# Kernel optimization log

Measured on AMD Instinct MI355X. Metric: run time of the kernel, lower is better.

Reference implementation:

```python
import jax, jax.numpy as jnp
import numpy as np

TOP_K = 2
EPS = 1e-10


def setup_inputs() -> dict:
    key = jax.random.key(0)
    k1, k2, k3, k4 = jax.random.split(key, 4)
    B, S, H, E = 4, 2048, 1024, 8
    tokens = jax.random.normal(k1, (B, S, H), dtype=jnp.float32)
    router_w = jax.random.normal(k2, (E, H), dtype=jnp.float32) * (1.0 / np.sqrt(H))
    router_b = jax.random.normal(k3, (E,), dtype=jnp.float32) * 0.01
    expert_weights = jax.random.normal(k4, (E, H, H), dtype=jnp.float32) * (1.0 / np.sqrt(H))
    return {"tokens": tokens, "router_w": router_w, "router_b": router_b,
            "expert_weights": expert_weights}


def reference(tokens, router_w, router_b, expert_weights):
    B, S, H = tokens.shape
    E = expert_weights.shape[0]
    # Router (torch Linear: x @ W^T + b)
    logits = jnp.einsum('bsh,eh->bse', tokens, router_w) + router_b  # [B,S,E]
    probs = jax.nn.softmax(logits, axis=-1)
    top_p, top_i = jax.lax.top_k(probs, TOP_K)            # [B,S,K]
    w = top_p / (jnp.sum(top_p, axis=-1, keepdims=True) + EPS)  # normalized weights

    x = tokens.reshape(-1, H)                              # [N,H]
    idx = top_i.reshape(-1, TOP_K)                         # [N,K]
    wf = w.reshape(-1, TOP_K)                              # [N,K]

    # Expert GEMM: compute all experts then gather selected (dense, vectorized
    # equivalent of the sort/pad/grouped-GEMM dispatch; padded rows with
    # original_indices==-1 never contribute to the output).
    y_all = jnp.einsum('nh,ehd->ned', x, expert_weights)   # [N,E,H]
    y_k = jnp.take_along_axis(y_all, idx[:, :, None], axis=1)  # [N,K,H]

    out = jnp.einsum('nk,nkh->nh', wf, y_k)                # weighted combine
    acc = jnp.clip(jnp.sum(wf, axis=-1), EPS, None)        # weight accumulator
    out = (out / acc[:, None]).reshape(B, S, H)

    # epsilon scale tying output to normalized router probs (gradient path)
    scale = 1.0 + jnp.sum(w, axis=-1, keepdims=True) * EPS  # [B,S,1]
    return out * scale
```

## Files before the change

### kernel.cpp

```cpp
#include <hip/hip_runtime.h>
#include <stdint.h>

#define N_TOK 8192
#define H_DIM 1024
#define N_EXP 8
#define GEMM_GRID 1024

typedef __bf16 bf16x8 __attribute__((ext_vector_type(8)));
typedef float floatx4 __attribute__((ext_vector_type(4)));

typedef __attribute__((address_space(1))) void GV;
typedef __attribute__((address_space(3))) void LV;

static __device__ __forceinline__ unsigned short f2b(float f) {
    union { float f; unsigned int i; } v; v.f = f;
    unsigned int u = v.i;
    return (unsigned short)((u + 0x7FFFu + ((u >> 16) & 1u)) >> 16);
}
static __device__ __forceinline__ float b2f(unsigned short u) {
    union { unsigned int i; float f; } v; v.i = ((unsigned int)u) << 16; return v.f;
}

__global__ __launch_bounds__(256) void k_front(
    const float* __restrict__ tokens,
    const float* __restrict__ router_w,
    const float* __restrict__ router_b,
    const float* __restrict__ W,
    float* __restrict__ w_arr,
    unsigned short* __restrict__ tokb,
    unsigned short* __restrict__ Bp,
    int* __restrict__ cnt, int* __restrict__ bucket)
{
    const int t = threadIdx.x;

    if (blockIdx.x >= 1024) {
        const int idx = blockIdx.x - 1024;
        const int kg = idx & 127;
        const int e  = idx >> 7;
        const int d  = t * 4;
        const float* src = W + ((size_t)e * H_DIM + kg * 8) * H_DIM + d;
        float col[8][4];
#pragma unroll
        for (int j = 0; j < 8; ++j) {
            float4 v = *(const float4*)(src + (size_t)j * H_DIM);
            col[j][0] = v.x; col[j][1] = v.y; col[j][2] = v.z; col[j][3] = v.w;
        }
        unsigned short* dst = Bp + ((size_t)(e * 128 + kg) * H_DIM + d) * 8;
#pragma unroll
        for (int k = 0; k < 4; ++k) {
            unsigned short v[8];
#pragma unroll
            for (int j = 0; j < 8; ++j) v[j] = f2b(col[j][k]);
            *(uint4*)(dst + (size_t)k * 8) = *(uint4*)v;
        }
        return;
    }

    __shared__ int bcnt[N_EXP];
    __shared__ int blist[N_EXP][16];
    if (t < N_EXP) bcnt[t] = 0;
    __syncthreads();

    const int wv = t >> 6, lane = t & 63;
    const int n0 = blockIdx.x * 8 + wv * 2;

    float x0[16], x1[16];
    const float* xp0 = tokens + (size_t)n0 * H_DIM + lane * 16;
    const float* xp1 = xp0 + H_DIM;
#pragma unroll
    for (int i = 0; i < 4; ++i) {
        float4 v = *(const float4*)(xp0 + i * 4);
        x0[i * 4 + 0] = v.x; x0[i * 4 + 1] = v.y; x0[i * 4 + 2] = v.z; x0[i * 4 + 3] = v.w;
        float4 u = *(const float4*)(xp1 + i * 4);
        x1[i * 4 + 0] = u.x; x1[i * 4 + 1] = u.y; x1[i * 4 + 2] = u.z; x1[i * 4 + 3] = u.w;
    }
    {
        unsigned short xb[16];
#pragma unroll
        for (int j = 0; j < 16; ++j) xb[j] = f2b(x0[j]);
        unsigned short* dp = tokb + (size_t)n0 * H_DIM + lane * 16;
        *(uint4*)(dp) = *(uint4*)(xb); *(uint4*)(dp + 8) = *(uint4*)(xb + 8);
#pragma unroll
        for (int j = 0; j < 16; ++j) xb[j] = f2b(x1[j]);
        dp += H_DIM;
        *(uint4*)(dp) = *(uint4*)(xb); *(uint4*)(dp + 8) = *(uint4*)(xb + 8);
    }

    float a0[N_EXP], a1[N_EXP];
#pragma unroll
    for (int e = 0; e < N_EXP; ++e) {
        const float* wp = router_w + e * H_DIM + lane * 16;
        float s0 = 0.f, s1 = 0.f;
#pragma unroll
        for (int i = 0; i < 4; ++i) {
            float4 v = *(const float4*)(wp + i * 4);
            s0 += x0[i * 4 + 0] * v.x + x0[i * 4 + 1] * v.y + x0[i * 4 + 2] * v.z + x0[i * 4 + 3] * v.w;
            s1 += x1[i * 4 + 0] * v.x + x1[i * 4 + 1] * v.y + x1[i * 4 + 2] * v.z + x1[i * 4 + 3] * v.w;
        }
        a0[e] = s0; a1[e] = s1;
    }
#pragma unroll
    for (int e = 0; e < N_EXP; ++e) {
        float p = a0[e], q = a1[e];
#pragma unroll
        for (int off = 32; off > 0; off >>= 1) { p += __shfl_xor(p, off); q += __shfl_xor(q, off); }
        a0[e] = p; a1[e] = q;
    }

    if (lane == 0) {
#pragma unroll
        for (int k = 0; k < 2; ++k) {
            const int n = n0 + k;
            float lg[N_EXP];
#pragma unroll
            for (int e = 0; e < N_EXP; ++e) lg[e] = (k ? a1[e] : a0[e]) + router_b[e];
            int e0 = 0;
#pragma unroll
            for (int e = 1; e < N_EXP; ++e) if (lg[e] > lg[e0]) e0 = e;
            int e1 = -1;
#pragma unroll
            for (int e = 0; e < N_EXP; ++e) {
                if (e == e0) continue;
                if (e1 < 0 || lg[e] > lg[e1]) e1 = e;
            }
            float w0 = 1.f / (1.f + __expf(lg[e1] - lg[e0]));
            w_arr[n * 2] = w0;
            w_arr[n * 2 + 1] = 1.f - w0;
            int s0 = atomicAdd(&bcnt[e0], 1); blist[e0][s0] = 2 * n;
            int s1 = atomicAdd(&bcnt[e1], 1); blist[e1][s1] = 2 * n + 1;
        }
    }
    __syncthreads();

    if (t < N_EXP) {
        int c = bcnt[t];
        if (c > 0) {
            int base = atomicAdd(&cnt[t], c);
            int* dst = bucket + t * N_TOK + base;
            for (int i = 0; i < c; ++i) dst[i] = blist[t][i];
        }
    }
}

__global__ __launch_bounds__(256, 4) void k_gemm(
    const unsigned short* __restrict__ tokb,
    const unsigned short* __restrict__ Bp,
    const int* __restrict__ cnt, const int* __restrict__ bucket,
    unsigned short* __restrict__ Y, float* __restrict__ Yp, int split_ok)
{
    __shared__ __align__(16) unsigned short Asm[128 * 64];
    __shared__ __align__(16) unsigned short Bsm[8 * 128 * 8];
    __shared__ int rows[128];

    const int t = threadIdx.x;
    const int wv = t >> 6, lane = t & 63;
    const int w_row = wv >> 1, w_col = wv & 1;
    const int m_lane = lane & 15, quad = lane >> 4;
    const int r7 = m_lane & 7;
    const int p_sw = (lane & 7) ^ ((lane >> 3) & 7);

    int cs[N_EXP];
#pragma unroll
    for (int ee = 0; ee < N_EXP; ++ee) cs[ee] = cnt[ee];
    int T = 0;
#pragma unroll
    for (int ee = 0; ee < N_EXP; ++ee) T += (cs[ee] + 127) >> 7;

    const int x = blockIdx.x & 7;
    const int sblk = blockIdx.x >> 3;
    const int q = T >> 3, r = T & 7;
    const int tstart = (x < r) ? x * (q + 1) : r * (q + 1) + (x - r) * q;
    const int tcnt   = (x < r) ? (q + 1) : q;
    const int nloc   = tcnt * 8;

    int t0_tile, t0_nt, t0_k0, t0_k1, t0_os;
    int t1_tile = -1, t1_nt = 0, t1_k0 = 0, t1_k1 = 0, t1_os = -1;
    if (split_ok) {
        if (x < r && sblk < 32) {
            const int oi = sblk >> 2, qk = sblk & 3;
            t0_tile = tstart + 16; t0_nt = oi;
            t0_k0 = qk * 4; t0_k1 = qk * 4 + 4;
            t0_os = (x * 8 + oi) * 4 + qk;
            t1_tile = tstart + (sblk >> 3); t1_nt = sblk & 7;
            t1_k0 = 0; t1_k1 = 16; t1_os = -1;
        } else {
            t0_tile = tstart + (sblk >> 3); t0_nt = sblk & 7;
            t0_k0 = 0; t0_k1 = 16; t0_os = -1;
        }
    } else {
        t0_tile = tstart + (sblk >> 3); t0_nt = sblk & 7;
        t0_k0 = 0; t0_k1 = 16; t0_os = -1;
        if (sblk + 128 < nloc) {
            const int l2 = sblk + 128;
            t1_tile = tstart + (l2 >> 3); t1_nt = l2 & 7;
            t1_k0 = 0; t1_k1 = 16; t1_os = -1;
        }
    }

#pragma unroll 2
    for (int tk = 0; tk < 2; ++tk) {
        const int tile = tk ? t1_tile : t0_tile;
        if (tile < 0) continue;
        const int nt = tk ? t1_nt : t0_nt;
        const int k0 = tk ? t1_k0 : t0_k0;
        const int k1 = tk ? t1_k1 : t0_k1;
        const int os = tk ? t1_os : t0_os;

        int base = 0, e = 0, mt = 0;
#pragma unroll
        for (int ee = 0; ee < N_EXP; ++ee) {
            int te = (cs[ee] + 127) >> 7;
            if (tile >= base && tile < base + te) { e = ee; mt = tile - base; }
            base += te;
        }
        const int cnt_local = cs[e] - mt * 128;
        const int d0 = nt * 128;

        __syncthreads();
        if (t < 128)
            rows[t] = (t < cnt_local) ? bucket[e * N_TOK + mt * 128 + t] : -1;
        __syncthreads();

        const unsigned short* aptr[4];
#pragma unroll
        for (int i = 0; i < 4; ++i) {
            int rr = i * 32 + wv * 8 + (lane >> 3);
            int rid = rows[rr];
            int tok = (rid >= 0) ? (rid >> 1) : 0;
            aptr[i] = tokb + (size_t)tok * H_DIM + p_sw * 8;
        }
        const unsigned short* bbase = Bp
            + ((size_t)(e * 128 + (t >> 7)) * H_DIM + d0 + (t & 127)) * 8;

        floatx4 acc[4][4];
#pragma unroll
        for (int i = 0; i < 4; ++i)
#pragma unroll
            for (int j = 0; j < 4; ++j) acc[i][j] = (floatx4){0.f, 0.f, 0.f, 0.f};

        for (int kt = k0; kt < k1; ++kt) {
#pragma unroll
            for (int i = 0; i < 4; ++i) {
                __builtin_amdgcn_global_load_lds(
                    (GV*)(aptr[i] + kt * 64),
                    (LV*)(&Asm[i * 2048 + wv * 512]), 16, 0, 0);
                __builtin_amdgcn_global_load_lds(
                    (GV*)(bbase + (size_t)i * 16384 + (size_t)kt * 65536),
                    (LV*)(&Bsm[i * 2048 + wv * 512]), 16, 0, 0);
            }
            __syncthreads();

#pragma unroll
            for (int s = 0; s < 2; ++s) {
                bf16x8 a[4], b[4];
#pragma unroll
                for (int i = 0; i < 4; ++i) {
                    int row = w_row * 64 + i * 16 + m_lane;
                    a[i] = *(const bf16x8*)&Asm[row * 64 + ((s * 4 + quad) ^ r7) * 8];
                }
#pragma unroll
                for (int j = 0; j < 4; ++j)
                    b[j] = *(const bf16x8*)&Bsm[((s * 4 + quad) * 128 + w_col * 64 + j * 16 + m_lane) * 8];
#pragma unroll
                for (int i = 0; i < 4; ++i)
#pragma unroll
                    for (int j = 0; j < 4; ++j)
                        acc[i][j] = __builtin_amdgcn_mfma_f32_16x16x32_bf16(a[i], b[j], acc[i][j], 0, 0, 0);
            }
            __syncthreads();
        }

        if (os < 0) {
#pragma unroll
            for (int i = 0; i < 4; ++i) {
                const int lr_base = w_row * 64 + i * 16 + quad * 4;
#pragma unroll
                for (int reg = 0; reg < 4; ++reg) {
                    const int lr = lr_base + reg;
                    const int rid = rows[lr];
                    if (rid >= 0) {
                        unsigned short v[4];
#pragma unroll
                        for (int j = 0; j < 4; ++j) v[j] = f2b(acc[i][j][reg]);
                        *(uint2*)(Y + (size_t)rid * H_DIM + d0 + w_col * 64 + m_lane * 4) = *(uint2*)v;
                    }
                }
            }
        } else {
            float* dst = Yp + (size_t)os * 16384;
#pragma unroll
            for (int i = 0; i < 4; ++i) {
#pragma unroll
                for (int reg = 0; reg < 4; ++reg) {
                    const int lr = w_row * 64 + i * 16 + quad * 4 + reg;
                    float4 v = make_float4(acc[i][0][reg], acc[i][1][reg],
                                           acc[i][2][reg], acc[i][3][reg]);
                    *(float4*)(dst + lr * 128 + w_col * 64 + m_lane * 4) = v;
                }
            }
        }
    }
}

__global__ __launch_bounds__(256) void k_fix(
    const int* __restrict__ cnt, const int* __restrict__ bucket,
    const float* __restrict__ Yp, unsigned short* __restrict__ Y)
{
    int cs[N_EXP];
#pragma unroll
    for (int ee = 0; ee < N_EXP; ++ee) cs[ee] = cnt[ee];
    int T = 0;
#pragma unroll
    for (int ee = 0; ee < N_EXP; ++ee) T += (cs[ee] + 127) >> 7;
    const int q = T >> 3, r = T & 7;
    const int o = blockIdx.x;
    if (o >= 8 * r) return;
    const int x = o >> 3, oi = o & 7;
    const int tile = x * (q + 1) + q;
    const int nt = oi;

    int base = 0, e = 0, mt = 0;
#pragma unroll
    for (int ee = 0; ee < N_EXP; ++ee) {
        int te = (cs[ee] + 127) >> 7;
        if (tile >= base && tile < base + te) { e = ee; mt = tile - base; }
        base += te;
    }
    const int cnt_local = cs[e] - mt * 128;
    const int d0 = nt * 128;

    const int t = threadIdx.x;
    const int lr = t >> 1, half = t & 1;
    const int rid = (lr < cnt_local) ? bucket[e * N_TOK + mt * 128 + lr] : -1;
    if (rid < 0) return;

    const float* s = Yp + (size_t)o * 4 * 16384 + lr * 128 + half * 64;
    unsigned short* dst = Y + (size_t)rid * H_DIM + d0 + half * 64;
#pragma unroll
    for (int c = 0; c < 64; c += 8) {
        float sum[8];
#pragma unroll
        for (int k = 0; k < 8; ++k) sum[k] = s[c + k];
#pragma unroll
        for (int qk = 1; qk < 4; ++qk) {
            const float* sq = s + qk * 16384;
#pragma unroll
            for (int k = 0; k < 8; ++k) sum[k] += sq[c + k];
        }
        unsigned short v[8];
#pragma unroll
        for (int k = 0; k < 8; ++k) v[k] = f2b(sum[k]);
        *(uint4*)(dst + c) = *(uint4*)v;
    }
}

__global__ __launch_bounds__(256) void k_combine(
    const unsigned short* __restrict__ Y, const float* __restrict__ w_arr,
    float* __restrict__ out)
{
    __shared__ __align__(16) unsigned short Ys[4 * H_DIM];
    const int t = threadIdx.x;
    const int b = blockIdx.x;
    const int wv = t >> 6, lane = t & 63;
    const unsigned short* src = Y + (size_t)b * 4 * H_DIM;
#pragma unroll
    for (int r = 0; r < 2; ++r) {
        __builtin_amdgcn_global_load_lds(
            (GV*)(src + (size_t)r * 2048 + wv * 512 + lane * 8),
            (LV*)(&Ys[r * 2048 + wv * 512]), 16, 0, 0);
    }
    __syncthreads();

    const int tok = t >> 7;
    const int n = 2 * b + tok;
    const int d0 = (t & 127) * 8;
    const int seg = d0 >> 7;
    const int dseg = d0 & 127;
    const int wc = dseg >> 6;
    const int j  = (dseg >> 4) & 3;
    const int m0 = dseg & 15;
    const int sbase = tok * 2 * H_DIM + seg * 128 + wc * 64 + j;
    const float w0 = w_arr[2 * n], w1 = w_arr[2 * n + 1];

    float o[8];
#pragma unroll
    for (int k = 0; k < 8; ++k) {
        int s = sbase + (m0 + k) * 4;
        o[k] = w0 * b2f(Ys[s]) + w1 * b2f(Ys[s + H_DIM]);
    }
    float4* op = (float4*)(out + (size_t)n * H_DIM + d0);
    op[0] = make_float4(o[0], o[1], o[2], o[3]);
    op[1] = make_float4(o[4], o[5], o[6], o[7]);
}

extern "C" void kernel_launch(void* const* d_in, const int* in_sizes, int n_in,
                              void* d_out, int out_size, void* d_ws, size_t ws_size,
                              hipStream_t stream)
{
    const float* tokens   = (const float*)d_in[0];
    const float* router_w = (const float*)d_in[1];
    const float* router_b = (const float*)d_in[2];
    const float* W        = (const float*)d_in[3];
    float* out = (float*)d_out;

    char* ws = (char*)d_ws;
    int*   cnt    = (int*)(ws);
    float* w_arr  = (float*)(ws + 34816);
    int*   bucket = (int*)(ws + 100352);
    unsigned short* tokb = (unsigned short*)(ws + 362496);
    unsigned short* Bp   = (unsigned short*)(ws + 17139712);
    unsigned short* Y    = (unsigned short*)(ws + 33916928);
    float* Yp = (float*)(ws + 67471360);

    const int split_ok = (ws_size >= 82151424ull) ? 1 : 0;

    hipMemsetAsync(cnt, 0, N_EXP * sizeof(int), stream);
    k_front  <<<2048, 256, 0, stream>>>(tokens, router_w, router_b, W,
                                        w_arr, tokb, Bp, cnt, bucket);
    k_gemm   <<<GEMM_GRID, 256, 0, stream>>>(tokb, Bp, cnt, bucket, Y, Yp, split_ok);
    if (split_ok)
        k_fix<<<56, 256, 0, stream>>>(cnt, bucket, Yp, Y);
    k_combine<<<N_TOK * (H_DIM / 8) / 256, 256, 0, stream>>>(Y, w_arr, out);
}
```

Baseline: 190.0 us.

## Fold split-K partial reduction into combine kernel via per-row fix map

Removes the separate k_fix kernel that summed the four split-K fp32 partials and wrote them back to the bf16 Y buffer. The GEMM now records, for each row handled by a split tile, which partial buffer holds it. The combine kernel consults this map and reads and sums the fp32 partials directly instead of the bf16 Y values. This saves one kernel launch and a round-trip through Y, at the cost of an extra map read per token and a divergent branch in the combine kernel. As a side effect, split rows now skip bf16 rounding.

```diff
diff --git a/kernel.cpp b/kernel.cpp
--- a/kernel.cpp
+++ b/kernel.cpp
@@ -29,7 +29,8 @@
     float* __restrict__ w_arr,
     unsigned short* __restrict__ tokb,
     unsigned short* __restrict__ Bp,
-    int* __restrict__ cnt, int* __restrict__ bucket)
+    int* __restrict__ cnt, int* __restrict__ bucket,
+    int* __restrict__ fix_map)
 {
     const int t = threadIdx.x;
 
@@ -55,6 +56,8 @@
         }
         return;
     }
+
+    if (fix_map && t < 16) fix_map[blockIdx.x * 16 + t] = -1;
 
     __shared__ int bcnt[N_EXP];
     __shared__ int blist[N_EXP][16];
@@ -146,7 +149,8 @@
     const unsigned short* __restrict__ tokb,
     const unsigned short* __restrict__ Bp,
     const int* __restrict__ cnt, const int* __restrict__ bucket,
-    unsigned short* __restrict__ Y, float* __restrict__ Yp, int split_ok)
+    unsigned short* __restrict__ Y, float* __restrict__ Yp,
+    int* __restrict__ fix_map, int split_ok)
 {
     __shared__ __align__(16) unsigned short Asm[128 * 64];
     __shared__ __align__(16) unsigned short Bsm[8 * 128 * 8];
@@ -221,6 +225,9 @@
             rows[t] = (t < cnt_local) ? bucket[e * N_TOK + mt * 128 + t] : -1;
         __syncthreads();
 
+        if (os >= 0 && (os & 3) == 0 && t < 128 && rows[t] >= 0)
+            fix_map[rows[t]] = (x << 16) | t;
+
         const unsigned short* aptr[4];
 #pragma unroll
         for (int i = 0; i < 4; ++i) {
@@ -302,60 +309,9 @@
     }
 }
 
-__global__ __launch_bounds__(256) void k_fix(
-    const int* __restrict__ cnt, const int* __restrict__ bucket,
-    const float* __restrict__ Yp, unsigned short* __restrict__ Y)
-{
-    int cs[N_EXP];
-#pragma unroll
-    for (int ee = 0; ee < N_EXP; ++ee) cs[ee] = cnt[ee];
-    int T = 0;
-#pragma unroll
-    for (int ee = 0; ee < N_EXP; ++ee) T += (cs[ee] + 127) >> 7;
-    const int q = T >> 3, r = T & 7;
-    const int o = blockIdx.x;
-    if (o >= 8 * r) return;
-    const int x = o >> 3, oi = o & 7;
-    const int tile = x * (q + 1) + q;
-    const int nt = oi;
-
-    int base = 0, e = 0, mt = 0;
-#pragma unroll
-    for (int ee = 0; ee < N_EXP; ++ee) {
-        int te = (cs[ee] + 127) >> 7;
-        if (tile >= base && tile < base + te) { e = ee; mt = tile - base; }
-        base += te;
-    }
-    const int cnt_local = cs[e] - mt * 128;
-    const int d0 = nt * 128;
-
-    const int t = threadIdx.x;
-    const int lr = t >> 1, half = t & 1;
-    const int rid = (lr < cnt_local) ? bucket[e * N_TOK + mt * 128 + lr] : -1;
-    if (rid < 0) return;
-
-    const float* s = Yp + (size_t)o * 4 * 16384 + lr * 128 + half * 64;
-    unsigned short* dst = Y + (size_t)rid * H_DIM + d0 + half * 64;
-#pragma unroll
-    for (int c = 0; c < 64; c += 8) {
-        float sum[8];
-#pragma unroll
-        for (int k = 0; k < 8; ++k) sum[k] = s[c + k];
-#pragma unroll
-        for (int qk = 1; qk < 4; ++qk) {
-            const float* sq = s + qk * 16384;
-#pragma unroll
-            for (int k = 0; k < 8; ++k) sum[k] += sq[c + k];
-        }
-        unsigned short v[8];
-#pragma unroll
-        for (int k = 0; k < 8; ++k) v[k] = f2b(sum[k]);
-        *(uint4*)(dst + c) = *(uint4*)v;
-    }
-}
-
 __global__ __launch_bounds__(256) void k_combine(
     const unsigned short* __restrict__ Y, const float* __restrict__ w_arr,
+    const float* __restrict__ Yp, const int* __restrict__ fix_map,
     float* __restrict__ out)
 {
     __shared__ __align__(16) unsigned short Ys[4 * H_DIM];
@@ -379,15 +335,44 @@
     const int wc = dseg >> 6;
     const int j  = (dseg >> 4) & 3;
     const int m0 = dseg & 15;
-    const int sbase = tok * 2 * H_DIM + seg * 128 + wc * 64 + j;
+    const int tok2H = tok * 2 * H_DIM;
     const float w0 = w_arr[2 * n], w1 = w_arr[2 * n + 1];
 
+    const int rid0 = 4 * b + 2 * tok;
+    const int fm0 = fix_map ? fix_map[rid0] : -1;
+    const int fm1 = fix_map ? fix_map[rid0 + 1] : -1;
+
+    float v0[8], v1[8];
+    if (fm0 < 0) {
+#pragma unroll
+        for (int k = 0; k < 8; ++k)
+            v0[k] = b2f(Ys[tok2H + seg * 128 + wc * 64 + (m0 + k) * 4 + j]);
+    } else {
+        const float* yb = Yp + (size_t)(((fm0 >> 16) * 8 + seg) * 4) * 16384
+                             + (fm0 & 0xFFFF) * 128;
+#pragma unroll
+        for (int k = 0; k < 8; ++k) {
+            int sl = wc * 64 + (m0 + k) * 4 + j;
+            v0[k] = yb[sl] + yb[16384 + sl] + yb[32768 + sl] + yb[49152 + sl];
+        }
+    }
+    if (fm1 < 0) {
+#pragma unroll
+        for (int k = 0; k < 8; ++k)
+            v1[k] = b2f(Ys[tok2H + H_DIM + seg * 128 + wc * 64 + (m0 + k) * 4 + j]);
+    } else {
+        const float* yb = Yp + (size_t)(((fm1 >> 16) * 8 + seg) * 4) * 16384
+                             + (fm1 & 0xFFFF) * 128;
+#pragma unroll
+        for (int k = 0; k < 8; ++k) {
+            int sl = wc * 64 + (m0 + k) * 4 + j;
+            v1[k] = yb[sl] + yb[16384 + sl] + yb[32768 + sl] + yb[49152 + sl];
+        }
+    }
+
     float o[8];
 #pragma unroll
-    for (int k = 0; k < 8; ++k) {
-        int s = sbase + (m0 + k) * 4;
-        o[k] = w0 * b2f(Ys[s]) + w1 * b2f(Ys[s + H_DIM]);
-    }
+    for (int k = 0; k < 8; ++k) o[k] = w0 * v0[k] + w1 * v1[k];
     float4* op = (float4*)(out + (size_t)n * H_DIM + d0);
     op[0] = make_float4(o[0], o[1], o[2], o[3]);
     op[1] = make_float4(o[4], o[5], o[6], o[7]);
@@ -410,15 +395,15 @@
     unsigned short* tokb = (unsigned short*)(ws + 362496);
     unsigned short* Bp   = (unsigned short*)(ws + 17139712);
     unsigned short* Y    = (unsigned short*)(ws + 33916928);
-    float* Yp = (float*)(ws + 67471360);
-
-    const int split_ok = (ws_size >= 82151424ull) ? 1 : 0;
+    int*   fix_map = (int*)(ws + 67471360);
+    float* Yp      = (float*)(ws + 67536896);
+
+    const int split_ok = (ws_size >= 82216960ull) ? 1 : 0;
+    int* fm = split_ok ? fix_map : (int*)nullptr;
 
     hipMemsetAsync(cnt, 0, N_EXP * sizeof(int), stream);
     k_front  <<<2048, 256, 0, stream>>>(tokens, router_w, router_b, W,
-                                        w_arr, tokb, Bp, cnt, bucket);
-    k_gemm   <<<GEMM_GRID, 256, 0, stream>>>(tokb, Bp, cnt, bucket, Y, Yp, split_ok);
-    if (split_ok)
-        k_fix<<<56, 256, 0, stream>>>(cnt, bucket, Yp, Y);
-    k_combine<<<N_TOK * (H_DIM / 8) / 256, 256, 0, stream>>>(Y, w_arr, out);
-}
+                                        w_arr, tokb, Bp, cnt, bucket, fm);
+    k_gemm   <<<GEMM_GRID, 256, 0, stream>>>(tokb, Bp, cnt, bucket, Y, Yp, fm, split_ok);
+    k_combine<<<N_TOK * (H_DIM / 8) / 256, 256, 0, stream>>>(Y, w_arr, Yp, fm, out);
+}
```

Measured after the change: 177.5 us. -6.6%, faster.
